# Kernel tuning notes

Hardware: AMD Instinct MI355X
Metric: run time of the kernel (lower is better)

The kernel has to match this reference:

```python
import jax, jax.numpy as jnp
import numpy as np

# Staggered-grid first-derivative coefficients (Taylor-optimal), order -> c_1..c_N
_COEFFS = {2: (1.0,),
           4: (9.0 / 8.0, -1.0 / 24.0),
           6: (75.0 / 64.0, -25.0 / 384.0, 3.0 / 640.0),
           8: (1225.0 / 1024.0, -245.0 / 3072.0, 49.0 / 5120.0, -5.0 / 7168.0)}


def _shift(a, s, axis):
    """Zero-padded shift: out[i] = a[i + s] where valid, else 0."""
    if s == 0:
        return a
    nd = a.ndim
    sl = [slice(None)] * nd
    pad = [(0, 0)] * nd
    if s > 0:
        sl[axis] = slice(s, None)
        pad[axis] = (0, s)
    else:
        sl[axis] = slice(None, s)
        pad[axis] = (-s, 0)
    return jnp.pad(a[tuple(sl)], pad)


def _diff1(a, stencil, rd, axis):
    """Integer-grid staggered derivative: sum_k c_k (a[i+k-1] - a[i-k]) * rd."""
    d = jnp.zeros_like(a)
    for k, ck in enumerate(_COEFFS[stencil], start=1):
        d = d + ck * (_shift(a, k - 1, axis) - _shift(a, -k, axis))
    return d * rd


def _diffh1(a, stencil, rd, axis):
    """Half-grid staggered derivative: sum_k c_k (a[i+k] - a[i-k+1]) * rd."""
    d = jnp.zeros_like(a)
    for k, ck in enumerate(_COEFFS[stencil], start=1):
        d = d + ck * (_shift(a, k, axis) - _shift(a, -(k - 1), axis))
    return d * rd


def _step(ca, cb, cq, Ey, Hx, Hz, m_Hx_z, m_Hz_x, m_Ey_x, m_Ey_z,
          ky, ky_h, ay, ay_h, by, by_h, kx, kx_h, ax, ax_h, bx, bx_h,
          rdy, rdx, stencil):
    # ---- update_E ----
    dHz_dx = _diff1(Hz, stencil, rdx, -1)   # d/dx along last axis
    dHx_dz = _diff1(Hx, stencil, rdy, -2)   # d/dz (y) along axis -2
    m_Hz_x = bx * m_Hz_x + ax * dHz_dx
    m_Hx_z = by * m_Hx_z + ay * dHx_dz
    Ey = ca * Ey + cb * ((dHz_dx / kx + m_Hz_x) - (dHx_dz / ky + m_Hx_z))
    # ---- update_H ----
    dEy_dz = _diffh1(Ey, stencil, rdy, -2)
    dEy_dx = _diffh1(Ey, stencil, rdx, -1)
    m_Ey_z = by_h * m_Ey_z + ay_h * dEy_dz
    m_Ey_x = bx_h * m_Ey_x + ax_h * dEy_dx
    Hx = Hx - cq * (dEy_dz / ky_h + m_Ey_z)
    Hz = Hz + cq * (dEy_dx / kx_h + m_Ey_x)
    return jnp.stack([Ey, Hx, Hz, m_Hx_z, m_Hz_x, m_Ey_x, m_Ey_z])


def setup_inputs() -> dict:
    B, NY, NX = 2, 2048, 2048
    key = jax.random.key(0)
    ks = jax.random.split(key, 25)
    f32 = jnp.float32

    def rn(k, s):
        return jax.random.normal(k, s, f32)

    def ru(k, s):
        return jax.random.uniform(k, s, f32)

    inp = {
        'ca': 0.9 + 0.1 * ru(ks[0], (NY, NX)),        # ~1 (low-loss media)
        'cb': 0.1 * ru(ks[1], (NY, NX)),
        'cq': 0.1 * ru(ks[2], (NY, NX)),
        'Ey': rn(ks[3], (B, NY, NX)),
        'Hx': rn(ks[4], (B, NY, NX)),
        'Hz': rn(ks[5], (B, NY, NX)),
        'm_Hx_z': rn(ks[6], (B, NY, NX)),
        'm_Hz_x': rn(ks[7], (B, NY, NX)),
        'm_Ey_x': rn(ks[8], (B, NY, NX)),
        'm_Ey_z': rn(ks[9], (B, NY, NX)),
        'ky': 1.0 + ru(ks[10], (NY, 1)),              # kappa >= 1
        'ky_h': 1.0 + ru(ks[11], (NY, 1)),
        'ay': 0.1 * ru(ks[12], (NY, 1)),
        'ay_h': 0.1 * ru(ks[13], (NY, 1)),
        'by': 0.9 * ru(ks[14], (NY, 1)),
        'by_h': 0.9 * ru(ks[15], (NY, 1)),
        'kx': 1.0 + ru(ks[16], (NX,)),
        'kx_h': 1.0 + ru(ks[17], (NX,)),
        'ax': 0.1 * ru(ks[18], (NX,)),
        'ax_h': 0.1 * ru(ks[19], (NX,)),
        'bx': 0.9 * ru(ks[20], (NX,)),
        'bx_h': 0.9 * ru(ks[21], (NX,)),
        'rdy': jnp.float32(0.1),
        'rdx': jnp.float32(0.1),
        'stencil': 4,
    }
    return inp


def reference(ca, cb, cq, Ey, Hx, Hz, m_Hx_z, m_Hz_x, m_Ey_x, m_Ey_z,
              ky, ky_h, ay, ay_h, by, by_h, kx, kx_h, ax, ax_h, bx, bx_h,
              rdy, rdx, stencil):
    return _step(ca, cb, cq, Ey, Hx, Hz, m_Hx_z, m_Hz_x, m_Ey_x, m_Ey_z,
                 ky, ky_h, ay, ay_h, by, by_h, kx, kx_h, ax, ax_h, bx, bx_h,
                 rdy, rdx, int(stencil))
```

## Files before the change

### kernel.cpp

```cpp
#include <hip/hip_runtime.h>

typedef __attribute__((ext_vector_type(4))) float float4v;

__device__ __forceinline__ void getC(int st, float C[4]) {
    C[0] = 1.f; C[1] = 0.f; C[2] = 0.f; C[3] = 0.f;
    if (st == 4)      { C[0] = 1.125f;          C[1] = -1.f / 24.f; }
    else if (st == 6) { C[0] = 75.f / 64.f;     C[1] = -25.f / 384.f;
                        C[2] = 3.f / 640.f; }
    else if (st == 8) { C[0] = 1225.f / 1024.f; C[1] = -245.f / 3072.f;
                        C[2] = 49.f / 5120.f;   C[3] = -5.f / 7168.f; }
}

__device__ __forceinline__ void ld8(const float* __restrict__ p, float o[8]) {
    float4v a = *(const float4v*)p;
    float4v b = *(const float4v*)(p + 4);
    o[0] = a.x; o[1] = a.y; o[2] = a.z; o[3] = a.w;
    o[4] = b.x; o[5] = b.y; o[6] = b.z; o[7] = b.w;
}
__device__ __forceinline__ void st8(float* __restrict__ p, const float o[8]) {
    float4v a = { o[0], o[1], o[2], o[3] };
    float4v b = { o[4], o[5], o[6], o[7] };
    *(float4v*)p       = a;
    *(float4v*)(p + 4) = b;
}

__global__ __launch_bounds__(256) void k1_updateE(
    const float* __restrict__ ca, const float* __restrict__ cb,
    const float* __restrict__ Ey, const float* __restrict__ Hx,
    const float* __restrict__ Hz,
    const float* __restrict__ mHxz, const float* __restrict__ mHzx,
    const float* __restrict__ ky, const float* __restrict__ ay,
    const float* __restrict__ by,
    const float* __restrict__ kx, const float* __restrict__ ax,
    const float* __restrict__ bx,
    const float* __restrict__ rdyp, const float* __restrict__ rdxp,
    const int* __restrict__ stp,
    float* __restrict__ outEy, float* __restrict__ outMHxz,
    float* __restrict__ outMHzx,
    int B, int NY, int NX)
{
    constexpr int EPT = 8;
    const int y = blockIdx.x, b = blockIdx.y;
    const int x0 = (int)threadIdx.x * EPT;
    const size_t row  = ((size_t)b * NY + y) * (size_t)NX;
    const size_t crow = (size_t)y * (size_t)NX;

    const float rdx = rdxp[0];
    const float rdy = rdyp[0];
    int ns = stp[0] >> 1;
    if (ns < 1) ns = 1; if (ns > 4) ns = 4;
    float C[4]; getC(ns * 2, C);

    float w[16];
    {
        ld8(Hz + row + x0, &w[4]);
        #pragma unroll
        for (int j = 0; j < 4; ++j) {
            const int x = x0 - 4 + j;
            w[j] = (x >= 0 && j >= 4 - ns) ? Hz[row + x] : 0.f;
        }
        #pragma unroll
        for (int j = 12; j < 15; ++j) {
            const int x = x0 - 4 + j;
            w[j] = (x < NX && j <= 10 + ns) ? Hz[row + x] : 0.f;
        }
        w[15] = 0.f;
    }

    float dHzdx[EPT], dHxdz[EPT];
    #pragma unroll
    for (int i = 0; i < EPT; ++i) { dHzdx[i] = 0.f; dHxdz[i] = 0.f; }

    #pragma unroll
    for (int k = 1; k <= 4; ++k) {
        if (k <= ns) {
            const float ck = C[k - 1];
            #pragma unroll
            for (int i = 0; i < EPT; ++i)
                dHzdx[i] += ck * (w[i + 4 + k - 1] - w[i + 4 - k]);

            const int yp = y + k - 1, ym = y - k;
            float up[EPT], dn[EPT];
            if (yp < NY) {
                ld8(Hx + ((size_t)b * NY + yp) * (size_t)NX + x0, up);
            } else {
                #pragma unroll
                for (int i = 0; i < EPT; ++i) up[i] = 0.f;
            }
            if (ym >= 0) {
                ld8(Hx + ((size_t)b * NY + ym) * (size_t)NX + x0, dn);
            } else {
                #pragma unroll
                for (int i = 0; i < EPT; ++i) dn[i] = 0.f;
            }
            #pragma unroll
            for (int i = 0; i < EPT; ++i) dHxdz[i] += ck * (up[i] - dn[i]);
        }
    }

    float eyv[EPT], mzxv[EPT], mxzv[EPT], cav[EPT], cbv[EPT];
    float kxv[EPT], axv[EPT], bxv[EPT];
    ld8(Ey   + row + x0, eyv);
    ld8(mHzx + row + x0, mzxv);
    ld8(mHxz + row + x0, mxzv);
    ld8(ca + crow + x0, cav);
    ld8(cb + crow + x0, cbv);
    ld8(kx + x0, kxv);
    ld8(ax + x0, axv);
    ld8(bx + x0, bxv);
    const float kyv = ky[y];
    const float ayv = ay[y];
    const float byv = by[y];

    float oE[EPT], oMxz[EPT], oMzx[EPT];
    #pragma unroll
    for (int i = 0; i < EPT; ++i) {
        const float dzx = dHzdx[i] * rdx;
        const float dxz = dHxdz[i] * rdy;
        const float mzx_n = bxv[i] * mzxv[i] + axv[i] * dzx;
        const float mxz_n = byv * mxzv[i] + ayv * dxz;
        const float ey_n = cav[i] * eyv[i]
            + cbv[i] * ((dzx / kxv[i] + mzx_n) - (dxz / kyv + mxz_n));
        oE[i]   = ey_n;
        oMxz[i] = mxz_n;
        oMzx[i] = mzx_n;
    }
    st8(outEy   + row + x0, oE);
    st8(outMHxz + row + x0, oMxz);
    st8(outMHzx + row + x0, oMzx);
}

__global__ __launch_bounds__(256) void k2_updateH(
    const float* __restrict__ cq,
    const float* __restrict__ Hx, const float* __restrict__ Hz,
    const float* __restrict__ mEyx, const float* __restrict__ mEyz,
    const float* __restrict__ kyh, const float* __restrict__ ayh,
    const float* __restrict__ byh,
    const float* __restrict__ kxh, const float* __restrict__ axh,
    const float* __restrict__ bxh,
    const float* __restrict__ rdyp, const float* __restrict__ rdxp,
    const int* __restrict__ stp,
    const float* __restrict__ newEy,
    float* __restrict__ outHx, float* __restrict__ outHz,
    float* __restrict__ outMEyx, float* __restrict__ outMEyz,
    int B, int NY, int NX)
{
    constexpr int EPT = 8;
    const int y = blockIdx.x, b = blockIdx.y;
    const int x0 = (int)threadIdx.x * EPT;
    const size_t row  = ((size_t)b * NY + y) * (size_t)NX;
    const size_t crow = (size_t)y * (size_t)NX;

    const float rdx = rdxp[0];
    const float rdy = rdyp[0];
    int ns = stp[0] >> 1;
    if (ns < 1) ns = 1; if (ns > 4) ns = 4;
    float C[4]; getC(ns * 2, C);

    float w[16];
    w[0] = 0.f;
    {
        ld8(newEy + row + x0, &w[4]);
        #pragma unroll
        for (int j = 1; j < 4; ++j) {
            const int x = x0 - 4 + j;
            w[j] = (x >= 0 && j >= 5 - ns) ? newEy[row + x] : 0.f;
        }
        #pragma unroll
        for (int j = 12; j < 16; ++j) {
            const int x = x0 - 4 + j;
            w[j] = (x < NX && j <= 11 + ns) ? newEy[row + x] : 0.f;
        }
    }

    float dEdx[EPT], dEdz[EPT];
    #pragma unroll
    for (int i = 0; i < EPT; ++i) { dEdx[i] = 0.f; dEdz[i] = 0.f; }

    #pragma unroll
    for (int k = 1; k <= 4; ++k) {
        if (k <= ns) {
            const float ck = C[k - 1];
            #pragma unroll
            for (int i = 0; i < EPT; ++i)
                dEdx[i] += ck * (w[i + 4 + k] - w[i + 5 - k]);

            const int yp = y + k, ym = y + 1 - k;
            float up[EPT], dn[EPT];
            if (yp < NY) {
                ld8(newEy + ((size_t)b * NY + yp) * (size_t)NX + x0, up);
            } else {
                #pragma unroll
                for (int i = 0; i < EPT; ++i) up[i] = 0.f;
            }
            if (k == 1) {
                #pragma unroll
                for (int i = 0; i < EPT; ++i) dn[i] = w[4 + i];
            } else if (ym >= 0) {
                ld8(newEy + ((size_t)b * NY + ym) * (size_t)NX + x0, dn);
            } else {
                #pragma unroll
                for (int i = 0; i < EPT; ++i) dn[i] = 0.f;
            }
            #pragma unroll
            for (int i = 0; i < EPT; ++i) dEdz[i] += ck * (up[i] - dn[i]);
        }
    }

    float hxv[EPT], hzv[EPT], mxv[EPT], mzv[EPT], cqv[EPT];
    float kxhv[EPT], axhv[EPT], bxhv[EPT];
    ld8(Hx   + row + x0, hxv);
    ld8(Hz   + row + x0, hzv);
    ld8(mEyx + row + x0, mxv);
    ld8(mEyz + row + x0, mzv);
    ld8(cq + crow + x0, cqv);
    ld8(kxh + x0, kxhv);
    ld8(axh + x0, axhv);
    ld8(bxh + x0, bxhv);
    const float kyhv = kyh[y];
    const float ayhv = ayh[y];
    const float byhv = byh[y];

    float oHx[EPT], oHz[EPT], oMx[EPT], oMz[EPT];
    #pragma unroll
    for (int i = 0; i < EPT; ++i) {
        const float dz = dEdz[i] * rdy;
        const float dx = dEdx[i] * rdx;
        const float mz_n = byhv * mzv[i] + ayhv * dz;
        const float mx_n = bxhv[i] * mxv[i] + axhv[i] * dx;
        const float cqf = cqv[i];
        oHx[i] = hxv[i] - cqf * (dz / kyhv + mz_n);
        oHz[i] = hzv[i] + cqf * (dx / kxhv[i] + mx_n);
        oMx[i] = mx_n;
        oMz[i] = mz_n;
    }
    st8(outHx   + row + x0, oHx);
    st8(outHz   + row + x0, oHz);
    st8(outMEyx + row + x0, oMx);
    st8(outMEyz + row + x0, oMz);
}

extern "C" void kernel_launch(void* const* d_in, const int* in_sizes, int n_in,
                              void* d_out, int out_size, void* d_ws, size_t ws_size,
                              hipStream_t stream)
{
    const float* ca   = (const float*)d_in[0];
    const float* cb   = (const float*)d_in[1];
    const float* cq   = (const float*)d_in[2];
    const float* Ey   = (const float*)d_in[3];
    const float* Hx   = (const float*)d_in[4];
    const float* Hz   = (const float*)d_in[5];
    const float* mHxz = (const float*)d_in[6];
    const float* mHzx = (const float*)d_in[7];
    const float* mEyx = (const float*)d_in[8];
    const float* mEyz = (const float*)d_in[9];
    const float* ky   = (const float*)d_in[10];
    const float* kyh  = (const float*)d_in[11];
    const float* ay   = (const float*)d_in[12];
    const float* ayh  = (const float*)d_in[13];
    const float* by   = (const float*)d_in[14];
    const float* byh  = (const float*)d_in[15];
    const float* kx   = (const float*)d_in[16];
    const float* kxh  = (const float*)d_in[17];
    const float* ax   = (const float*)d_in[18];
    const float* axh  = (const float*)d_in[19];
    const float* bx   = (const float*)d_in[20];
    const float* bxh  = (const float*)d_in[21];
    const float* rdy  = (const float*)d_in[22];
    const float* rdx  = (const float*)d_in[23];
    const int* stp    = (const int*)d_in[24];

    const int NX   = in_sizes[16];
    const int NYNX = in_sizes[0];
    const int NY   = NYNX / NX;
    const int B    = in_sizes[3] / NYNX;
    const size_t plane = (size_t)B * (size_t)NYNX;

    float* out     = (float*)d_out;
    float* outEy   = out;
    float* outHx   = out + 1 * plane;
    float* outHz   = out + 2 * plane;
    float* outMHxz = out + 3 * plane;
    float* outMHzx = out + 4 * plane;
    float* outMEyx = out + 5 * plane;
    float* outMEyz = out + 6 * plane;

    dim3 grid(NY, B);
    dim3 block(NX / 8);

    k1_updateE<<<grid, block, 0, stream>>>(
        ca, cb, Ey, Hx, Hz, mHxz, mHzx, ky, ay, by, kx, ax, bx,
        rdy, rdx, stp, outEy, outMHxz, outMHzx, B, NY, NX);

    k2_updateH<<<grid, block, 0, stream>>>(
        cq, Hx, Hz, mEyx, mEyz, kyh, ayh, byh, kxh, axh, bxh,
        rdy, rdx, stp, outEy, outHx, outHz, outMEyx, outMEyz,
        B, NY, NX);
}
```

Measured before the change: 516.7 us.

## Fuse E and H updates into one kernel with LDS ring buffer of Ey rows

Merges the two kernels into one. Each workgroup handles an 8-row strip by 1024-column chunk, computes new Ey rows (including halo rows recomputed redundantly), and keeps them in a shared-memory ring buffer. The H update then reads Ey from LDS instead of re-reading the written Ey from global memory. It also swaps divisions for hardware reciprocal approximations and remaps block indices to spread strips across XCDs. The cost is redundant halo E computation, barriers per row, and slight precision changes from rcp.

```diff
diff --git a/kernel.cpp b/kernel.cpp
--- a/kernel.cpp
+++ b/kernel.cpp
@@ -1,6 +1,21 @@
 #include <hip/hip_runtime.h>
 
 typedef __attribute__((ext_vector_type(4))) float float4v;
+
+#define TY    8
+#define CXW   1024
+#define CXP   (CXW + 8)
+#define NSLOT 8
+
+__device__ __forceinline__ float4v ld4(const float* __restrict__ p) {
+    return *(const float4v*)p;
+}
+__device__ __forceinline__ void st4(float* __restrict__ p, float4v v) {
+    *(float4v*)p = v;
+}
+__device__ __forceinline__ float frcp(float x) {
+    return __builtin_amdgcn_rcpf(x);
+}
 
 __device__ __forceinline__ void getC(int st, float C[4]) {
     C[0] = 1.f; C[1] = 0.f; C[2] = 0.f; C[3] = 0.f;
@@ -11,39 +26,44 @@
                         C[2] = 49.f / 5120.f;   C[3] = -5.f / 7168.f; }
 }
 
-__device__ __forceinline__ void ld8(const float* __restrict__ p, float o[8]) {
-    float4v a = *(const float4v*)p;
-    float4v b = *(const float4v*)(p + 4);
-    o[0] = a.x; o[1] = a.y; o[2] = a.z; o[3] = a.w;
-    o[4] = b.x; o[5] = b.y; o[6] = b.z; o[7] = b.w;
-}
-__device__ __forceinline__ void st8(float* __restrict__ p, const float o[8]) {
-    float4v a = { o[0], o[1], o[2], o[3] };
-    float4v b = { o[4], o[5], o[6], o[7] };
-    *(float4v*)p       = a;
-    *(float4v*)(p + 4) = b;
-}
-
-__global__ __launch_bounds__(256) void k1_updateE(
-    const float* __restrict__ ca, const float* __restrict__ cb,
-    const float* __restrict__ Ey, const float* __restrict__ Hx,
+__global__ __launch_bounds__(256) void fdtd_fused(
+    const float* __restrict__ ca,   const float* __restrict__ cb,
+    const float* __restrict__ cq,
+    const float* __restrict__ Ey,   const float* __restrict__ Hx,
     const float* __restrict__ Hz,
     const float* __restrict__ mHxz, const float* __restrict__ mHzx,
-    const float* __restrict__ ky, const float* __restrict__ ay,
-    const float* __restrict__ by,
-    const float* __restrict__ kx, const float* __restrict__ ax,
-    const float* __restrict__ bx,
+    const float* __restrict__ mEyx, const float* __restrict__ mEyz,
+    const float* __restrict__ ky,   const float* __restrict__ kyh,
+    const float* __restrict__ ay,   const float* __restrict__ ayh,
+    const float* __restrict__ by,   const float* __restrict__ byh,
+    const float* __restrict__ kx,   const float* __restrict__ kxh,
+    const float* __restrict__ ax,   const float* __restrict__ axh,
+    const float* __restrict__ bx,   const float* __restrict__ bxh,
     const float* __restrict__ rdyp, const float* __restrict__ rdxp,
     const int* __restrict__ stp,
-    float* __restrict__ outEy, float* __restrict__ outMHxz,
-    float* __restrict__ outMHzx,
-    int B, int NY, int NX)
+    float* __restrict__ outEy,   float* __restrict__ outHx,
+    float* __restrict__ outHz,   float* __restrict__ outMHxz,
+    float* __restrict__ outMHzx, float* __restrict__ outMEyx,
+    float* __restrict__ outMEyz,
+    int B, int NY, int NX, int NSTRIP, int NCHUNK)
 {
-    constexpr int EPT = 8;
-    const int y = blockIdx.x, b = blockIdx.y;
-    const int x0 = (int)threadIdx.x * EPT;
-    const size_t row  = ((size_t)b * NY + y) * (size_t)NX;
-    const size_t crow = (size_t)y * (size_t)NX;
+    __shared__ float eyl[NSLOT][CXP];
+
+    const int nwg = NSTRIP * NCHUNK;
+    int idx = blockIdx.x;
+    if ((nwg & 7) == 0) {
+        const int q = nwg >> 3;
+        idx = (idx & 7) * q + (idx >> 3);
+    }
+    const int strip = idx % NSTRIP;
+    const int chunk = idx / NSTRIP;
+    const int b   = blockIdx.y;
+    const int y0  = strip * TY;
+    const int X0  = chunk * CXW;
+
+    const int tid = (int)threadIdx.x;
+    const int x0  = X0 + tid * 4;
+    const int lc0 = tid * 4;
 
     const float rdx = rdxp[0];
     const float rdy = rdyp[0];
@@ -51,193 +71,153 @@
     if (ns < 1) ns = 1; if (ns > 4) ns = 4;
     float C[4]; getC(ns * 2, C);
 
-    float w[16];
-    {
-        ld8(Hz + row + x0, &w[4]);
+    const size_t NXs = (size_t)NX;
+    const size_t planeOff = (size_t)b * (size_t)NY * NXs;
+    const float4v z4 = {0.f, 0.f, 0.f, 0.f};
+
+    float4v kxhv = z4, axhv = z4, bxhv = z4, rkxh = z4;
+    if (x0 + 4 <= NX) {
+        kxhv = ld4(kxh + x0); axhv = ld4(axh + x0); bxhv = ld4(bxh + x0);
         #pragma unroll
-        for (int j = 0; j < 4; ++j) {
-            const int x = x0 - 4 + j;
-            w[j] = (x >= 0 && j >= 4 - ns) ? Hz[row + x] : 0.f;
-        }
+        for (int i = 0; i < 4; ++i) rkxh[i] = frcp(kxhv[i]);
+    }
+
+    auto computeE = [&](int r, int xb, bool wr,
+                        float ayv, float byv, float rky) -> float4v {
+        if (r < 0 || r >= NY || xb < 0 || xb >= NX) return z4;
+        const size_t rb = planeOff + (size_t)r * NXs;
+        float w[12];
+        {
+            float4v l0 = (xb >= 4)       ? ld4(Hz + rb + (xb - 4)) : z4;
+            float4v l1 =                   ld4(Hz + rb + xb);
+            float4v l2 = (xb + 8 <= NX)  ? ld4(Hz + rb + xb + 4)   : z4;
+            w[0]=l0.x; w[1]=l0.y; w[2] =l0.z; w[3] =l0.w;
+            w[4]=l1.x; w[5]=l1.y; w[6] =l1.z; w[7] =l1.w;
+            w[8]=l2.x; w[9]=l2.y; w[10]=l2.z; w[11]=l2.w;
+        }
+        float dzx[4] = {0.f,0.f,0.f,0.f}, dxz[4] = {0.f,0.f,0.f,0.f};
         #pragma unroll
-        for (int j = 12; j < 15; ++j) {
-            const int x = x0 - 4 + j;
-            w[j] = (x < NX && j <= 10 + ns) ? Hz[row + x] : 0.f;
-        }
-        w[15] = 0.f;
+        for (int k = 1; k <= 4; ++k) {
+            if (k <= ns) {
+                const float ck = C[k - 1];
+                #pragma unroll
+                for (int i = 0; i < 4; ++i)
+                    dzx[i] += ck * (w[i + 3 + k] - w[i + 4 - k]);
+                const int yp = r + k - 1, ym = r - k;
+                float4v up = (yp < NY) ? ld4(Hx + rb + (size_t)(k - 1) * NXs + xb) : z4;
+                float4v dn = (ym >= 0) ? ld4(Hx + rb - (size_t)k * NXs + xb)       : z4;
+                #pragma unroll
+                for (int i = 0; i < 4; ++i)
+                    dxz[i] += ck * (up[i] - dn[i]);
+            }
+        }
+        const size_t cr = (size_t)r * NXs + (size_t)xb;
+        float4v eyv = ld4(Ey   + rb + xb);
+        float4v mzx = ld4(mHzx + rb + xb);
+        float4v mxz = ld4(mHxz + rb + xb);
+        float4v cav = ld4(ca + cr);
+        float4v cbv = ld4(cb + cr);
+        float4v kxv = ld4(kx + xb);
+        float4v axv = ld4(ax + xb);
+        float4v bxv = ld4(bx + xb);
+        float4v oE, oMxz, oMzx;
+        #pragma unroll
+        for (int i = 0; i < 4; ++i) {
+            const float dHzdx = dzx[i] * rdx;
+            const float dHxdz = dxz[i] * rdy;
+            const float mzx_n = bxv[i] * mzx[i] + axv[i] * dHzdx;
+            const float mxz_n = byv    * mxz[i] + ayv    * dHxdz;
+            oE[i] = cav[i] * eyv[i]
+                  + cbv[i] * ((dHzdx * frcp(kxv[i]) + mzx_n)
+                            - (dHxdz * rky          + mxz_n));
+            oMxz[i] = mxz_n;
+            oMzx[i] = mzx_n;
+        }
+        if (wr) {
+            st4(outEy   + rb + xb, oE);
+            st4(outMHxz + rb + xb, oMxz);
+            st4(outMHzx + rb + xb, oMzx);
+        }
+        return oE;
+    };
+
+    for (int e = 1 - ns; e < TY + ns; ++e) {
+        const int r = y0 + e;
+        float ayv = 0.f, byv = 0.f, rky = 0.f;
+        if (r >= 0 && r < NY) {
+            ayv = ay[r]; byv = by[r]; rky = frcp(ky[r]);
+        }
+        const bool wr = (e >= 0) && (e < TY);
+        float4v eM = computeE(r, x0, wr, ayv, byv, rky);
+        float4v eL = z4, eR = z4;
+        if (tid == 0 && X0 >= 4)
+            eL = computeE(r, X0 - 4, false, ayv, byv, rky);
+        if (tid == 255 && X0 + CXW < NX)
+            eR = computeE(r, X0 + CXW, false, ayv, byv, rky);
+
+        __syncthreads();
+        const int slot = r & (NSLOT - 1);
+        st4(&eyl[slot][lc0 + 4], eM);
+        if (tid == 0)   st4(&eyl[slot][0],        eL);
+        if (tid == 255) st4(&eyl[slot][CXW + 4],  eR);
+        __syncthreads();
+
+        if (e >= ns) {
+            const int h = r - ns;
+            if (h < NY && x0 + 4 <= NX) {
+                const size_t rb = planeOff + (size_t)h * NXs;
+                const int hs = h & (NSLOT - 1);
+                float lw[12];
+                {
+                    float4v a0 = ld4(&eyl[hs][lc0]);
+                    float4v a1 = ld4(&eyl[hs][lc0 + 4]);
+                    float4v a2 = ld4(&eyl[hs][lc0 + 8]);
+                    lw[0]=a0.x; lw[1]=a0.y; lw[2] =a0.z; lw[3] =a0.w;
+                    lw[4]=a1.x; lw[5]=a1.y; lw[6] =a1.z; lw[7] =a1.w;
+                    lw[8]=a2.x; lw[9]=a2.y; lw[10]=a2.z; lw[11]=a2.w;
+                }
+                float dEdx[4] = {0.f,0.f,0.f,0.f}, dEdz[4] = {0.f,0.f,0.f,0.f};
+                #pragma unroll
+                for (int k = 1; k <= 4; ++k) {
+                    if (k <= ns) {
+                        const float ck = C[k - 1];
+                        #pragma unroll
+                        for (int i = 0; i < 4; ++i)
+                            dEdx[i] += ck * (lw[i + 4 + k] - lw[i + 5 - k]);
+                        float4v up = ld4(&eyl[(h + k)     & (NSLOT - 1)][lc0 + 4]);
+                        float4v dn = ld4(&eyl[(h - k + 1) & (NSLOT - 1)][lc0 + 4]);
+                        #pragma unroll
+                        for (int i = 0; i < 4; ++i)
+                            dEdz[i] += ck * (up[i] - dn[i]);
+                    }
+                }
+                float4v hxv = ld4(Hx   + rb + x0);
+                float4v hzv = ld4(Hz   + rb + x0);
+                float4v mxv = ld4(mEyx + rb + x0);
+                float4v mzv = ld4(mEyz + rb + x0);
+                float4v cqv = ld4(cq + (size_t)h * NXs + x0);
+                const float ayhv = ayh[h];
+                const float byhv = byh[h];
+                const float rkyh = frcp(kyh[h]);
+                float4v oHx, oHz, oMx, oMz;
+                #pragma unroll
+                for (int i = 0; i < 4; ++i) {
+                    const float dz = dEdz[i] * rdy;
+                    const float dx = dEdx[i] * rdx;
+                    const float mz_n = byhv    * mzv[i] + ayhv    * dz;
+                    const float mx_n = bxhv[i] * mxv[i] + axhv[i] * dx;
+                    oHx[i] = hxv[i] - cqv[i] * (dz * rkyh    + mz_n);
+                    oHz[i] = hzv[i] + cqv[i] * (dx * rkxh[i] + mx_n);
+                    oMx[i] = mx_n;
+                    oMz[i] = mz_n;
+                }
+                st4(outHx   + rb + x0, oHx);
+                st4(outHz   + rb + x0, oHz);
+                st4(outMEyx + rb + x0, oMx);
+                st4(outMEyz + rb + x0, oMz);
+            }
+        }
     }
-
-    float dHzdx[EPT], dHxdz[EPT];
-    #pragma unroll
-    for (int i = 0; i < EPT; ++i) { dHzdx[i] = 0.f; dHxdz[i] = 0.f; }
-
-    #pragma unroll
-    for (int k = 1; k <= 4; ++k) {
-        if (k <= ns) {
-            const float ck = C[k - 1];
-            #pragma unroll
-            for (int i = 0; i < EPT; ++i)
-                dHzdx[i] += ck * (w[i + 4 + k - 1] - w[i + 4 - k]);
-
-            const int yp = y + k - 1, ym = y - k;
-            float up[EPT], dn[EPT];
-            if (yp < NY) {
-                ld8(Hx + ((size_t)b * NY + yp) * (size_t)NX + x0, up);
-            } else {
-                #pragma unroll
-                for (int i = 0; i < EPT; ++i) up[i] = 0.f;
-            }
-            if (ym >= 0) {
-                ld8(Hx + ((size_t)b * NY + ym) * (size_t)NX + x0, dn);
-            } else {
-                #pragma unroll
-                for (int i = 0; i < EPT; ++i) dn[i] = 0.f;
-            }
-            #pragma unroll
-            for (int i = 0; i < EPT; ++i) dHxdz[i] += ck * (up[i] - dn[i]);
-        }
-    }
-
-    float eyv[EPT], mzxv[EPT], mxzv[EPT], cav[EPT], cbv[EPT];
-    float kxv[EPT], axv[EPT], bxv[EPT];
-    ld8(Ey   + row + x0, eyv);
-    ld8(mHzx + row + x0, mzxv);
-    ld8(mHxz + row + x0, mxzv);
-    ld8(ca + crow + x0, cav);
-    ld8(cb + crow + x0, cbv);
-    ld8(kx + x0, kxv);
-    ld8(ax + x0, axv);
-    ld8(bx + x0, bxv);
-    const float kyv = ky[y];
-    const float ayv = ay[y];
-    const float byv = by[y];
-
-    float oE[EPT], oMxz[EPT], oMzx[EPT];
-    #pragma unroll
-    for (int i = 0; i < EPT; ++i) {
-        const float dzx = dHzdx[i] * rdx;
-        const float dxz = dHxdz[i] * rdy;
-        const float mzx_n = bxv[i] * mzxv[i] + axv[i] * dzx;
-        const float mxz_n = byv * mxzv[i] + ayv * dxz;
-        const float ey_n = cav[i] * eyv[i]
-            + cbv[i] * ((dzx / kxv[i] + mzx_n) - (dxz / kyv + mxz_n));
-        oE[i]   = ey_n;
-        oMxz[i] = mxz_n;
-        oMzx[i] = mzx_n;
-    }
-    st8(outEy   + row + x0, oE);
-    st8(outMHxz + row + x0, oMxz);
-    st8(outMHzx + row + x0, oMzx);
-}
-
-__global__ __launch_bounds__(256) void k2_updateH(
-    const float* __restrict__ cq,
-    const float* __restrict__ Hx, const float* __restrict__ Hz,
-    const float* __restrict__ mEyx, const float* __restrict__ mEyz,
-    const float* __restrict__ kyh, const float* __restrict__ ayh,
-    const float* __restrict__ byh,
-    const float* __restrict__ kxh, const float* __restrict__ axh,
-    const float* __restrict__ bxh,
-    const float* __restrict__ rdyp, const float* __restrict__ rdxp,
-    const int* __restrict__ stp,
-    const float* __restrict__ newEy,
-    float* __restrict__ outHx, float* __restrict__ outHz,
-    float* __restrict__ outMEyx, float* __restrict__ outMEyz,
-    int B, int NY, int NX)
-{
-    constexpr int EPT = 8;
-    const int y = blockIdx.x, b = blockIdx.y;
-    const int x0 = (int)threadIdx.x * EPT;
-    const size_t row  = ((size_t)b * NY + y) * (size_t)NX;
-    const size_t crow = (size_t)y * (size_t)NX;
-
-    const float rdx = rdxp[0];
-    const float rdy = rdyp[0];
-    int ns = stp[0] >> 1;
-    if (ns < 1) ns = 1; if (ns > 4) ns = 4;
-    float C[4]; getC(ns * 2, C);
-
-    float w[16];
-    w[0] = 0.f;
-    {
-        ld8(newEy + row + x0, &w[4]);
-        #pragma unroll
-        for (int j = 1; j < 4; ++j) {
-            const int x = x0 - 4 + j;
-            w[j] = (x >= 0 && j >= 5 - ns) ? newEy[row + x] : 0.f;
-        }
-        #pragma unroll
-        for (int j = 12; j < 16; ++j) {
-            const int x = x0 - 4 + j;
-            w[j] = (x < NX && j <= 11 + ns) ? newEy[row + x] : 0.f;
-        }
-    }
-
-    float dEdx[EPT], dEdz[EPT];
-    #pragma unroll
-    for (int i = 0; i < EPT; ++i) { dEdx[i] = 0.f; dEdz[i] = 0.f; }
-
-    #pragma unroll
-    for (int k = 1; k <= 4; ++k) {
-        if (k <= ns) {
-            const float ck = C[k - 1];
-            #pragma unroll
-            for (int i = 0; i < EPT; ++i)
-                dEdx[i] += ck * (w[i + 4 + k] - w[i + 5 - k]);
-
-            const int yp = y + k, ym = y + 1 - k;
-            float up[EPT], dn[EPT];
-            if (yp < NY) {
-                ld8(newEy + ((size_t)b * NY + yp) * (size_t)NX + x0, up);
-            } else {
-                #pragma unroll
-                for (int i = 0; i < EPT; ++i) up[i] = 0.f;
-            }
-            if (k == 1) {
-                #pragma unroll
-                for (int i = 0; i < EPT; ++i) dn[i] = w[4 + i];
-            } else if (ym >= 0) {
-                ld8(newEy + ((size_t)b * NY + ym) * (size_t)NX + x0, dn);
-            } else {
-                #pragma unroll
-                for (int i = 0; i < EPT; ++i) dn[i] = 0.f;
-            }
-            #pragma unroll
-            for (int i = 0; i < EPT; ++i) dEdz[i] += ck * (up[i] - dn[i]);
-        }
-    }
-
-    float hxv[EPT], hzv[EPT], mxv[EPT], mzv[EPT], cqv[EPT];
-    float kxhv[EPT], axhv[EPT], bxhv[EPT];
-    ld8(Hx   + row + x0, hxv);
-    ld8(Hz   + row + x0, hzv);
-    ld8(mEyx + row + x0, mxv);
-    ld8(mEyz + row + x0, mzv);
-    ld8(cq + crow + x0, cqv);
-    ld8(kxh + x0, kxhv);
-    ld8(axh + x0, axhv);
-    ld8(bxh + x0, bxhv);
-    const float kyhv = kyh[y];
-    const float ayhv = ayh[y];
-    const float byhv = byh[y];
-
-    float oHx[EPT], oHz[EPT], oMx[EPT], oMz[EPT];
-    #pragma unroll
-    for (int i = 0; i < EPT; ++i) {
-        const float dz = dEdz[i] * rdy;
-        const float dx = dEdx[i] * rdx;
-        const float mz_n = byhv * mzv[i] + ayhv * dz;
-        const float mx_n = bxhv[i] * mxv[i] + axhv[i] * dx;
-        const float cqf = cqv[i];
-        oHx[i] = hxv[i] - cqf * (dz / kyhv + mz_n);
-        oHz[i] = hzv[i] + cqf * (dx / kxhv[i] + mx_n);
-        oMx[i] = mx_n;
-        oMz[i] = mz_n;
-    }
-    st8(outHx   + row + x0, oHx);
-    st8(outHz   + row + x0, oHz);
-    st8(outMEyx + row + x0, oMx);
-    st8(outMEyz + row + x0, oMz);
 }
 
 extern "C" void kernel_launch(void* const* d_in, const int* in_sizes, int n_in,
@@ -268,7 +248,7 @@
     const float* bxh  = (const float*)d_in[21];
     const float* rdy  = (const float*)d_in[22];
     const float* rdx  = (const float*)d_in[23];
-    const int* stp    = (const int*)d_in[24];
+    const int*   stp  = (const int*)d_in[24];
 
     const int NX   = in_sizes[16];
     const int NYNX = in_sizes[0];
@@ -285,15 +265,16 @@
     float* outMEyx = out + 5 * plane;
     float* outMEyz = out + 6 * plane;
 
-    dim3 grid(NY, B);
-    dim3 block(NX / 8);
-
-    k1_updateE<<<grid, block, 0, stream>>>(
-        ca, cb, Ey, Hx, Hz, mHxz, mHzx, ky, ay, by, kx, ax, bx,
-        rdy, rdx, stp, outEy, outMHxz, outMHzx, B, NY, NX);
-
-    k2_updateH<<<grid, block, 0, stream>>>(
-        cq, Hx, Hz, mEyx, mEyz, kyh, ayh, byh, kxh, axh, bxh,
-        rdy, rdx, stp, outEy, outHx, outHz, outMEyx, outMEyz,
-        B, NY, NX);
-}
+    const int NSTRIP = (NY + TY - 1) / TY;
+    const int NCHUNK = (NX + CXW - 1) / CXW;
+
+    dim3 grid(NSTRIP * NCHUNK, B);
+    dim3 block(256);
+
+    fdtd_fused<<<grid, block, 0, stream>>>(
+        ca, cb, cq, Ey, Hx, Hz, mHxz, mHzx, mEyx, mEyz,
+        ky, kyh, ay, ayh, by, byh, kx, kxh, ax, axh, bx, bxh,
+        rdy, rdx, stp,
+        outEy, outHx, outHz, outMHxz, outMHzx, outMEyx, outMEyz,
+        B, NY, NX, NSTRIP, NCHUNK);
+}
```

Result: faster. 501.4 us (-3.0%).
